# Kernel tuning notes

Measured on AMD Instinct MI355X. Metric: run time of the kernel, lower is better.

The kernel has to match this reference:

```python
import jax, jax.numpy as jnp
import numpy as np

V = 196608   # HEALPix nside=128 pixels
NNZ = 9 * V  # ~8 neighbors + self loop per pixel
B, FIN, FOUT, K = 4, 32, 64, 5


def setup_inputs() -> dict:
    key = jax.random.key(0)
    k1, k2, k3, k4, k5, k6 = jax.random.split(key, 6)
    lap_rows = jax.random.randint(k1, (NNZ,), 0, V, dtype=jnp.int32)
    lap_cols = jax.random.randint(k2, (NNZ,), 0, V, dtype=jnp.int32)
    # scale values so the Chebyshev recurrence stays numerically tame
    lap_vals = jax.random.normal(k3, (NNZ,), dtype=jnp.float32) * 0.1
    inputs = jax.random.normal(k4, (B, V, FIN), dtype=jnp.float32)
    std = np.sqrt(2.0 / (FIN + FOUT)).astype(np.float32)  # xavier normal
    weight = jax.random.normal(k5, (K, FIN, FOUT), dtype=jnp.float32) * std
    bias = jnp.full((FOUT,), 0.01, dtype=jnp.float32)
    return {"lap_rows": lap_rows, "lap_cols": lap_cols, "lap_vals": lap_vals,
            "inputs": inputs, "weight": weight, "bias": bias}


def reference(lap_rows, lap_cols, lap_vals, inputs, weight, bias):
    Bq, Vq, Fin = inputs.shape
    Kq, _, Fout = weight.shape

    # x0: [V, Fin*B]  (matches torch permute(1,2,0).reshape)
    x0 = jnp.transpose(inputs, (1, 2, 0)).reshape(Vq, Fin * Bq)

    def spmm(x):  # sparse [V,V] @ dense [V, Fin*B] via gather + scatter-add
        contrib = lap_vals[:, None] * x[lap_cols]  # [nnz, Fin*B]
        return jax.ops.segment_sum(contrib, lap_rows, num_segments=Vq)

    xs = [x0]
    if Kq > 1:
        xs.append(spmm(x0))
    for _ in range(2, Kq):
        xs.append(2.0 * spmm(xs[-1]) - xs[-2])
    cheb = jnp.stack(xs)  # [K, V, Fin*B]

    # [K,V,Fin,B] -> [B,V,Fin,K] -> [B*V, Fin*K]
    cheb = cheb.reshape(Kq, Vq, Fin, Bq).transpose(3, 1, 2, 0).reshape(Bq * Vq, Fin * Kq)
    # torch weight.view(Fin*K, Fout) flattens (K,Fin) row-major -> reshape(K*Fin, Fout)
    w2 = weight.reshape(Kq * Fin, Fout)
    out = (cheb @ w2).reshape(Bq, Vq, Fout)
    return out + bias
```

## Files before the change

### kernel.cpp

```cpp
#include <hip/hip_runtime.h>

#define V 196608
#define NNZ (9 * V)
#define B 4
#define FIN 32
#define FOUT 64
#define K 5
#define C 128
#define ROWU 64
#define SPMM_BLOCKS 2048

typedef __attribute__((ext_vector_type(8))) short bf16x8;
typedef __attribute__((ext_vector_type(4))) float f32x4;

static __device__ __forceinline__ unsigned int f2bf(float f) {
    union { float f; unsigned int u; } v; v.f = f;
    return (v.u + 0x7FFFu + ((v.u >> 16) & 1u)) >> 16;
}
static __device__ __forceinline__ float bflo(unsigned int u) {
    union { unsigned int u; float f; } v; v.u = u << 16; return v.f;
}
static __device__ __forceinline__ float bfhi(unsigned int u) {
    union { unsigned int u; float f; } v; v.u = u & 0xFFFF0000u; return v.f;
}

__global__ void zero_cursor(uint4* __restrict__ p) {
    int t = blockIdx.x * 256 + threadIdx.x;
    if (t < V / 4) p[t] = (uint4){0u, 0u, 0u, 0u};
}

__global__ void build_x0(const float* __restrict__ inp, unsigned int* __restrict__ x0) {
    int t = blockIdx.x * 256 + threadIdx.x;
    if (t >= V * 64) return;
    int d = t & 63;
    int v = t >> 6;
    int b = d >> 4;
    int fin = (d & 15) * 2;
    const float* s = inp + ((size_t)b * V + v) * 32 + fin;
    float f0 = s[0], f1 = s[1];
    x0[(size_t)v * ROWU + d] = f2bf(f0) | (f2bf(f1) << 16);
}

__global__ void build_wfrag(const float* __restrict__ w, uint4* __restrict__ wfh,
                            uint4* __restrict__ wfl) {
    int idx = blockIdx.x * 256 + threadIdx.x;
    if (idx >= K * 4 * 64) return;
    int lane = idx & 63;
    int nt = (idx >> 6) & 3;
    int k = idx >> 8;
    int col = lane & 15;
    int quad = lane >> 4;
    int o = nt * 16 + col;
    unsigned int hh[8], ll[8];
#pragma unroll
    for (int e = 0; e < 8; ++e) {
        int fin = quad * 8 + e;
        float wv = w[(fin * 5 + k) * 64 + o];
        unsigned int hb = f2bf(wv);
        float hf = bflo(hb);
        ll[e] = f2bf(wv - hf);
        hh[e] = hb;
    }
    uint4 uh, ul;
    uh.x = hh[0] | (hh[1] << 16);
    uh.y = hh[2] | (hh[3] << 16);
    uh.z = hh[4] | (hh[5] << 16);
    uh.w = hh[6] | (hh[7] << 16);
    ul.x = ll[0] | (ll[1] << 16);
    ul.y = ll[2] | (ll[3] << 16);
    ul.z = ll[4] | (ll[5] << 16);
    ul.w = ll[6] | (ll[7] << 16);
    wfh[idx] = uh;
    wfl[idx] = ul;
}

__global__ void hist_rows(const int* __restrict__ rows, int* __restrict__ cnt) {
    int e = blockIdx.x * 256 + threadIdx.x;
    if (e < NNZ) atomicAdd(&cnt[rows[e]], 1);
}

__global__ void chunk_sums(const int* __restrict__ cnt, int* __restrict__ bsum) {
    __shared__ int ws[16];
    int tid = threadIdx.x;
    int lane = tid & 63;
    int wid = tid >> 6;
    int v = cnt[blockIdx.x * 1024 + tid];
#pragma unroll
    for (int off = 32; off >= 1; off >>= 1) v += __shfl_down(v, off, 64);
    if (lane == 0) ws[wid] = v;
    __syncthreads();
    if (tid < 16) {
        int s = ws[tid];
#pragma unroll
        for (int off = 8; off >= 1; off >>= 1) s += __shfl_down(s, off, 16);
        if (tid == 0) bsum[blockIdx.x] = s;
    }
}

__global__ void scan_sums(const int* __restrict__ bsum, int* __restrict__ bpre,
                          int* __restrict__ rowptr) {
    __shared__ int ws[4];
    int tid = threadIdx.x;
    int lane = tid & 63;
    int wid = tid >> 6;
    int v = (tid < 192) ? bsum[tid] : 0;
    int x = v;
#pragma unroll
    for (int off = 1; off < 64; off <<= 1) {
        int t = __shfl_up(x, off, 64);
        if (lane >= off) x += t;
    }
    if (lane == 63) ws[wid] = x;
    __syncthreads();
    if (wid == 0 && lane < 4) {
        int s = ws[lane];
        int y = s;
#pragma unroll
        for (int off = 1; off < 4; off <<= 1) {
            int t = __shfl_up(y, off, 4);
            if (lane >= off) y += t;
        }
        ws[lane] = y - s;
    }
    __syncthreads();
    int incl = x + ws[wid];
    if (tid < 192) bpre[tid] = incl - v;
    if (tid == 191) rowptr[V] = incl;
}

__global__ void scan_chunks(const int* __restrict__ cnt, const int* __restrict__ bpre,
                            int* __restrict__ rowptr, int* __restrict__ cursor) {
    __shared__ int wsum[16];
    int tid = threadIdx.x;
    int lane = tid & 63;
    int wid = tid >> 6;
    int base = blockIdx.x * 1024;
    int v = cnt[base + tid];
    int x = v;
#pragma unroll
    for (int off = 1; off < 64; off <<= 1) {
        int t = __shfl_up(x, off, 64);
        if (lane >= off) x += t;
    }
    if (lane == 63) wsum[wid] = x;
    __syncthreads();
    if (wid == 0 && lane < 16) {
        int s = wsum[lane];
        int y = s;
#pragma unroll
        for (int off = 1; off < 16; off <<= 1) {
            int t = __shfl_up(y, off, 16);
            if (lane >= off) y += t;
        }
        wsum[lane] = y - s;
    }
    __syncthreads();
    int excl = x - v + wsum[wid] + bpre[blockIdx.x];
    rowptr[base + tid] = excl;
    cursor[base + tid] = excl;
}

__global__ void scatter_edges_win(const int* __restrict__ rows, const int* __restrict__ cols,
                                  const float* __restrict__ vals, int* __restrict__ cursor,
                                  int2* __restrict__ cev, int lo, int hi) {
    int e = blockIdx.x * 256 + threadIdx.x;
    if (e >= NNZ) return;
    int r = rows[e];
    if (r < lo || r >= hi) return;
    int p = atomicAdd(&cursor[r], 1);
    int2 pk;
    pk.x = cols[e];
    pk.y = __float_as_int(vals[e]);
    cev[p] = pk;
}

template <int COMBINE>
__global__ __launch_bounds__(256) void spmm_gather(
    const int* __restrict__ rowptr, const int2* __restrict__ cev,
    const unsigned int* __restrict__ x, const unsigned int* __restrict__ xm2,
    unsigned int* __restrict__ y) {
    const int lane = threadIdx.x & 63;
    const int wid0 = (blockIdx.x * 256 + threadIdx.x) >> 6;
    const int NW = SPMM_BLOCKS * 4;
    for (int base = wid0 * 2; base < V; base += NW * 2) {
        const int r0 = base, r1 = base + 1;
        const int s0 = rowptr[r0];
        const int e0 = rowptr[r0 + 1];
        const int e1 = rowptr[r1 + 1];
        float ax0 = 0.f, ay0 = 0.f, ax1 = 0.f, ay1 = 0.f;
        int i0 = s0, i1 = e0;
        while (e0 - i0 >= 4 && e1 - i1 >= 4) {
            int2 Ea[4], Eb[4];
#pragma unroll
            for (int j = 0; j < 4; ++j) {
                Ea[j] = cev[i0 + j];
                Eb[j] = cev[i1 + j];
            }
            unsigned int Ua[4], Ub[4];
#pragma unroll
            for (int j = 0; j < 4; ++j) {
                Ua[j] = x[(size_t)Ea[j].x * ROWU + lane];
                Ub[j] = x[(size_t)Eb[j].x * ROWU + lane];
            }
#pragma unroll
            for (int j = 0; j < 4; ++j) {
                float va = __int_as_float(Ea[j].y);
                float vb = __int_as_float(Eb[j].y);
                ax0 = fmaf(va, bflo(Ua[j]), ax0);
                ay0 = fmaf(va, bfhi(Ua[j]), ay0);
                ax1 = fmaf(vb, bflo(Ub[j]), ax1);
                ay1 = fmaf(vb, bfhi(Ub[j]), ay1);
            }
            i0 += 4;
            i1 += 4;
        }
        for (; i0 + 2 <= e0; i0 += 2) {
            int2 a = cev[i0], b = cev[i0 + 1];
            unsigned int u0 = x[(size_t)a.x * ROWU + lane];
            unsigned int u1 = x[(size_t)b.x * ROWU + lane];
            float v0 = __int_as_float(a.y), v1 = __int_as_float(b.y);
            ax0 = fmaf(v0, bflo(u0), ax0);
            ay0 = fmaf(v0, bfhi(u0), ay0);
            ax0 = fmaf(v1, bflo(u1), ax0);
            ay0 = fmaf(v1, bfhi(u1), ay0);
        }
        for (; i0 < e0; ++i0) {
            int2 a = cev[i0];
            unsigned int u = x[(size_t)a.x * ROWU + lane];
            float v = __int_as_float(a.y);
            ax0 = fmaf(v, bflo(u), ax0);
            ay0 = fmaf(v, bfhi(u), ay0);
        }
        for (; i1 + 2 <= e1; i1 += 2) {
            int2 a = cev[i1], b = cev[i1 + 1];
            unsigned int u0 = x[(size_t)a.x * ROWU + lane];
            unsigned int u1 = x[(size_t)b.x * ROWU + lane];
            float v0 = __int_as_float(a.y), v1 = __int_as_float(b.y);
            ax1 = fmaf(v0, bflo(u0), ax1);
            ay1 = fmaf(v0, bfhi(u0), ay1);
            ax1 = fmaf(v1, bflo(u1), ax1);
            ay1 = fmaf(v1, bfhi(u1), ay1);
        }
        for (; i1 < e1; ++i1) {
            int2 a = cev[i1];
            unsigned int u = x[(size_t)a.x * ROWU + lane];
            float v = __int_as_float(a.y);
            ax1 = fmaf(v, bflo(u), ax1);
            ay1 = fmaf(v, bfhi(u), ay1);
        }
        if (COMBINE) {
            unsigned int m0 = xm2[(size_t)r0 * ROWU + lane];
            unsigned int m1 = xm2[(size_t)r1 * ROWU + lane];
            ax0 = 2.0f * ax0 - bflo(m0);
            ay0 = 2.0f * ay0 - bfhi(m0);
            ax1 = 2.0f * ax1 - bflo(m1);
            ay1 = 2.0f * ay1 - bfhi(m1);
        }
        y[(size_t)r0 * ROWU + lane] = f2bf(ax0) | (f2bf(ay0) << 16);
        y[(size_t)r1 * ROWU + lane] = f2bf(ax1) | (f2bf(ay1) << 16);
    }
}

__global__ __launch_bounds__(256) void fused_mfma(
    const unsigned short* __restrict__ x0, const unsigned short* __restrict__ x1,
    const unsigned short* __restrict__ x2, const unsigned short* __restrict__ x3,
    const unsigned short* __restrict__ x4, const uint4* __restrict__ wfh,
    const uint4* __restrict__ wfl, const float* __restrict__ bias,
    float* __restrict__ out) {
    const int tid = threadIdx.x;
    const int lane = tid & 63;
    const int g = (blockIdx.x * 256 + tid) >> 6;
    const int v0 = g << 4;
    const int col = lane & 15;
    const int quad = lane >> 4;
    const unsigned short* const xs[K] = {x0, x1, x2, x3, x4};

    f32x4 acc[B][4];
#pragma unroll
    for (int b = 0; b < B; ++b)
#pragma unroll
        for (int nt = 0; nt < 4; ++nt) acc[b][nt] = (f32x4){0.f, 0.f, 0.f, 0.f};

#pragma unroll
    for (int k = 0; k < K; ++k) {
        const unsigned short* xk = xs[k] + ((size_t)(v0 + col)) * C + quad * 8;
        bf16x8 a0 = *reinterpret_cast<const bf16x8*>(xk);
        bf16x8 a1 = *reinterpret_cast<const bf16x8*>(xk + 32);
        bf16x8 a2 = *reinterpret_cast<const bf16x8*>(xk + 64);
        bf16x8 a3 = *reinterpret_cast<const bf16x8*>(xk + 96);
#pragma unroll
        for (int nt = 0; nt < 4; ++nt) {
            uint4 uh = wfh[(k * 4 + nt) * 64 + lane];
            uint4 ul = wfl[(k * 4 + nt) * 64 + lane];
            bf16x8 wh = *reinterpret_cast<bf16x8*>(&uh);
            bf16x8 wl = *reinterpret_cast<bf16x8*>(&ul);
            acc[0][nt] = __builtin_amdgcn_mfma_f32_16x16x32_bf16(a0, wh, acc[0][nt], 0, 0, 0);
            acc[1][nt] = __builtin_amdgcn_mfma_f32_16x16x32_bf16(a1, wh, acc[1][nt], 0, 0, 0);
            acc[2][nt] = __builtin_amdgcn_mfma_f32_16x16x32_bf16(a2, wh, acc[2][nt], 0, 0, 0);
            acc[3][nt] = __builtin_amdgcn_mfma_f32_16x16x32_bf16(a3, wh, acc[3][nt], 0, 0, 0);
            acc[0][nt] = __builtin_amdgcn_mfma_f32_16x16x32_bf16(a0, wl, acc[0][nt], 0, 0, 0);
            acc[1][nt] = __builtin_amdgcn_mfma_f32_16x16x32_bf16(a1, wl, acc[1][nt], 0, 0, 0);
            acc[2][nt] = __builtin_amdgcn_mfma_f32_16x16x32_bf16(a2, wl, acc[2][nt], 0, 0, 0);
            acc[3][nt] = __builtin_amdgcn_mfma_f32_16x16x32_bf16(a3, wl, acc[3][nt], 0, 0, 0);
        }
    }

    float bv[4];
#pragma unroll
    for (int nt = 0; nt < 4; ++nt) bv[nt] = bias[nt * 16 + col];
#pragma unroll
    for (int b = 0; b < B; ++b)
#pragma unroll
        for (int nt = 0; nt < 4; ++nt)
#pragma unroll
            for (int r = 0; r < 4; ++r) {
                int row = quad * 4 + r;
                out[((size_t)b * V + v0 + row) * FOUT + nt * 16 + col] = acc[b][nt][r] + bv[nt];
            }
}

extern "C" void kernel_launch(void* const* d_in, const int* in_sizes, int n_in,
                              void* d_out, int out_size, void* d_ws, size_t ws_size,
                              hipStream_t stream) {
    const int* lap_rows = (const int*)d_in[0];
    const int* lap_cols = (const int*)d_in[1];
    const float* lap_vals = (const float*)d_in[2];
    const float* inputs = (const float*)d_in[3];
    const float* weight = (const float*)d_in[4];
    const float* bias = (const float*)d_in[5];
    float* out = (float*)d_out;

    char* p = (char*)d_ws;
    auto alloc = [&](size_t bytes) {
        char* r = p;
        p += (bytes + 511) & ~(size_t)511;
        return r;
    };
    int* rowptr = (int*)alloc((size_t)(V + 1) * 4);
    int* cursor = (int*)alloc((size_t)V * 4);
    int* bsum = (int*)alloc(192 * 4);
    int* bpre = (int*)alloc(192 * 4);
    uint4* wfh = (uint4*)alloc((size_t)K * 4 * 64 * 16);
    uint4* wfl = (uint4*)alloc((size_t)K * 4 * 64 * 16);
    int2* cev = (int2*)alloc((size_t)NNZ * 8);
    unsigned int* xb0 = (unsigned int*)alloc((size_t)V * ROWU * 4);
    unsigned int* xb1 = (unsigned int*)alloc((size_t)V * ROWU * 4);
    unsigned int* xb2 = (unsigned int*)alloc((size_t)V * ROWU * 4);
    unsigned int* xb3 = (unsigned int*)alloc((size_t)V * ROWU * 4);
    unsigned int* xb4 = (unsigned int*)alloc((size_t)V * ROWU * 4);

    const int edge_blocks = (NNZ + 255) / 256;
    const int x0_blocks = (V * 64) / 256;
    const int mfma_blocks = (V / 16) * 64 / 256;

    zero_cursor<<<(V / 4 + 255) / 256, 256, 0, stream>>>((uint4*)cursor);
    hist_rows<<<edge_blocks, 256, 0, stream>>>(lap_rows, cursor);
    chunk_sums<<<V / 1024, 1024, 0, stream>>>(cursor, bsum);
    scan_sums<<<1, 256, 0, stream>>>(bsum, bpre, rowptr);
    scan_chunks<<<V / 1024, 1024, 0, stream>>>(cursor, bpre, rowptr, cursor);
    for (int w = 0; w < 4; ++w) {
        scatter_edges_win<<<edge_blocks, 256, 0, stream>>>(
            lap_rows, lap_cols, lap_vals, cursor, cev, w * (V / 4), (w + 1) * (V / 4));
    }

    build_x0<<<x0_blocks, 256, 0, stream>>>(inputs, xb0);
    build_wfrag<<<5, 256, 0, stream>>>(weight, wfh, wfl);

    spmm_gather<0><<<SPMM_BLOCKS, 256, 0, stream>>>(rowptr, cev, xb0, nullptr, xb1);
    spmm_gather<1><<<SPMM_BLOCKS, 256, 0, stream>>>(rowptr, cev, xb1, xb0, xb2);
    spmm_gather<1><<<SPMM_BLOCKS, 256, 0, stream>>>(rowptr, cev, xb2, xb1, xb3);
    spmm_gather<1><<<SPMM_BLOCKS, 256, 0, stream>>>(rowptr, cev, xb3, xb2, xb4);

    fused_mfma<<<mfma_blocks, 256, 0, stream>>>(
        (const unsigned short*)xb0, (const unsigned short*)xb1, (const unsigned short*)xb2,
        (const unsigned short*)xb3, (const unsigned short*)xb4, wfh, wfl, bias, out);
}
```

Measured before the change: 652.1 us.

## Partition SpMM work by equal nonzero ranges with binary-searched row bounds

Replaces the fixed two-rows-per-wave SpMM with a merge-path style kernel. Each wave gets a contiguous nnz range, locates its row bounds by binary search over rowptr, and streams edges eight at a time, flushing rows as boundaries pass. The aim is to balance work across waves, stream the edge array contiguously and keep eight gathers in flight. It adds binary-search overhead per wave and per-edge row-boundary checks.

```diff
diff --git a/kernel.cpp b/kernel.cpp
--- a/kernel.cpp
+++ b/kernel.cpp
@@ -175,89 +175,88 @@
 }
 
 template <int COMBINE>
-__global__ __launch_bounds__(256) void spmm_gather(
+__global__ __launch_bounds__(256) void spmm_seg(
     const int* __restrict__ rowptr, const int2* __restrict__ cev,
     const unsigned int* __restrict__ x, const unsigned int* __restrict__ xm2,
     unsigned int* __restrict__ y) {
     const int lane = threadIdx.x & 63;
-    const int wid0 = (blockIdx.x * 256 + threadIdx.x) >> 6;
+    const int w = (blockIdx.x * 256 + threadIdx.x) >> 6;
     const int NW = SPMM_BLOCKS * 4;
-    for (int base = wid0 * 2; base < V; base += NW * 2) {
-        const int r0 = base, r1 = base + 1;
-        const int s0 = rowptr[r0];
-        const int e0 = rowptr[r0 + 1];
-        const int e1 = rowptr[r1 + 1];
-        float ax0 = 0.f, ay0 = 0.f, ax1 = 0.f, ay1 = 0.f;
-        int i0 = s0, i1 = e0;
-        while (e0 - i0 >= 4 && e1 - i1 >= 4) {
-            int2 Ea[4], Eb[4];
-#pragma unroll
-            for (int j = 0; j < 4; ++j) {
-                Ea[j] = cev[i0 + j];
-                Eb[j] = cev[i1 + j];
+    const int lo = (int)((long long)NNZ * w / NW);
+    const int hi = (int)((long long)NNZ * (w + 1) / NW);
+    int a = 0, b = V;
+    while (a < b) {
+        int m = (a + b) >> 1;
+        if (rowptr[m] < lo) a = m + 1; else b = m;
+    }
+    int r = a;
+    int rend;
+    if (w == NW - 1) {
+        rend = V;
+    } else {
+        a = r; b = V;
+        while (a < b) {
+            int m = (a + b) >> 1;
+            if (rowptr[m] < hi) a = m + 1; else b = m;
+        }
+        rend = a;
+    }
+    if (r >= rend) return;
+    int i = rowptr[r];
+    const int e = rowptr[rend];
+    int nb = rowptr[r + 1];
+    float ax = 0.f, ay = 0.f;
+
+    auto flushrow = [&](int row) {
+        float ox = ax, oy = ay;
+        if (COMBINE) {
+            unsigned int m0 = xm2[(size_t)row * ROWU + lane];
+            ox = 2.f * ox - bflo(m0);
+            oy = 2.f * oy - bfhi(m0);
+        }
+        y[(size_t)row * ROWU + lane] = f2bf(ox) | (f2bf(oy) << 16);
+        ax = 0.f;
+        ay = 0.f;
+    };
+
+    while (i < e) {
+        if (e - i >= 8) {
+            int2 E8[8];
+#pragma unroll
+            for (int t = 0; t < 8; ++t) E8[t] = cev[i + t];
+            unsigned int U8[8];
+#pragma unroll
+            for (int t = 0; t < 8; ++t) U8[t] = x[(size_t)E8[t].x * ROWU + lane];
+#pragma unroll
+            for (int t = 0; t < 8; ++t) {
+                int cur = i + t;
+                while (cur == nb) {
+                    flushrow(r);
+                    ++r;
+                    nb = rowptr[r + 1];
+                }
+                float v = __int_as_float(E8[t].y);
+                ax = fmaf(v, bflo(U8[t]), ax);
+                ay = fmaf(v, bfhi(U8[t]), ay);
             }
-            unsigned int Ua[4], Ub[4];
-#pragma unroll
-            for (int j = 0; j < 4; ++j) {
-                Ua[j] = x[(size_t)Ea[j].x * ROWU + lane];
-                Ub[j] = x[(size_t)Eb[j].x * ROWU + lane];
+            i += 8;
+        } else {
+            int2 ev = cev[i];
+            unsigned int u = x[(size_t)ev.x * ROWU + lane];
+            while (i == nb) {
+                flushrow(r);
+                ++r;
+                nb = rowptr[r + 1];
             }
-#pragma unroll
-            for (int j = 0; j < 4; ++j) {
-                float va = __int_as_float(Ea[j].y);
-                float vb = __int_as_float(Eb[j].y);
-                ax0 = fmaf(va, bflo(Ua[j]), ax0);
-                ay0 = fmaf(va, bfhi(Ua[j]), ay0);
-                ax1 = fmaf(vb, bflo(Ub[j]), ax1);
-                ay1 = fmaf(vb, bfhi(Ub[j]), ay1);
-            }
-            i0 += 4;
-            i1 += 4;
-        }
-        for (; i0 + 2 <= e0; i0 += 2) {
-            int2 a = cev[i0], b = cev[i0 + 1];
-            unsigned int u0 = x[(size_t)a.x * ROWU + lane];
-            unsigned int u1 = x[(size_t)b.x * ROWU + lane];
-            float v0 = __int_as_float(a.y), v1 = __int_as_float(b.y);
-            ax0 = fmaf(v0, bflo(u0), ax0);
-            ay0 = fmaf(v0, bfhi(u0), ay0);
-            ax0 = fmaf(v1, bflo(u1), ax0);
-            ay0 = fmaf(v1, bfhi(u1), ay0);
-        }
-        for (; i0 < e0; ++i0) {
-            int2 a = cev[i0];
-            unsigned int u = x[(size_t)a.x * ROWU + lane];
-            float v = __int_as_float(a.y);
-            ax0 = fmaf(v, bflo(u), ax0);
-            ay0 = fmaf(v, bfhi(u), ay0);
-        }
-        for (; i1 + 2 <= e1; i1 += 2) {
-            int2 a = cev[i1], b = cev[i1 + 1];
-            unsigned int u0 = x[(size_t)a.x * ROWU + lane];
-            unsigned int u1 = x[(size_t)b.x * ROWU + lane];
-            float v0 = __int_as_float(a.y), v1 = __int_as_float(b.y);
-            ax1 = fmaf(v0, bflo(u0), ax1);
-            ay1 = fmaf(v0, bfhi(u0), ay1);
-            ax1 = fmaf(v1, bflo(u1), ax1);
-            ay1 = fmaf(v1, bfhi(u1), ay1);
-        }
-        for (; i1 < e1; ++i1) {
-            int2 a = cev[i1];
-            unsigned int u = x[(size_t)a.x * ROWU + lane];
-            float v = __int_as_float(a.y);
-            ax1 = fmaf(v, bflo(u), ax1);
-            ay1 = fmaf(v, bfhi(u), ay1);
-        }
-        if (COMBINE) {
-            unsigned int m0 = xm2[(size_t)r0 * ROWU + lane];
-            unsigned int m1 = xm2[(size_t)r1 * ROWU + lane];
-            ax0 = 2.0f * ax0 - bflo(m0);
-            ay0 = 2.0f * ay0 - bfhi(m0);
-            ax1 = 2.0f * ax1 - bflo(m1);
-            ay1 = 2.0f * ay1 - bfhi(m1);
-        }
-        y[(size_t)r0 * ROWU + lane] = f2bf(ax0) | (f2bf(ay0) << 16);
-        y[(size_t)r1 * ROWU + lane] = f2bf(ax1) | (f2bf(ay1) << 16);
+            float v = __int_as_float(ev.y);
+            ax = fmaf(v, bflo(u), ax);
+            ay = fmaf(v, bfhi(u), ay);
+            ++i;
+        }
+    }
+    while (r < rend) {
+        flushrow(r);
+        ++r;
     }
 }
 
@@ -366,10 +365,10 @@
     build_x0<<<x0_blocks, 256, 0, stream>>>(inputs, xb0);
     build_wfrag<<<5, 256, 0, stream>>>(weight, wfh, wfl);
 
-    spmm_gather<0><<<SPMM_BLOCKS, 256, 0, stream>>>(rowptr, cev, xb0, nullptr, xb1);
-    spmm_gather<1><<<SPMM_BLOCKS, 256, 0, stream>>>(rowptr, cev, xb1, xb0, xb2);
-    spmm_gather<1><<<SPMM_BLOCKS, 256, 0, stream>>>(rowptr, cev, xb2, xb1, xb3);
-    spmm_gather<1><<<SPMM_BLOCKS, 256, 0, stream>>>(rowptr, cev, xb3, xb2, xb4);
+    spmm_seg<0><<<SPMM_BLOCKS, 256, 0, stream>>>(rowptr, cev, xb0, nullptr, xb1);
+    spmm_seg<1><<<SPMM_BLOCKS, 256, 0, stream>>>(rowptr, cev, xb1, xb0, xb2);
+    spmm_seg<1><<<SPMM_BLOCKS, 256, 0, stream>>>(rowptr, cev, xb2, xb1, xb3);
+    spmm_seg<1><<<SPMM_BLOCKS, 256, 0, stream>>>(rowptr, cev, xb3, xb2, xb4);
 
     fused_mfma<<<mfma_blocks, 256, 0, stream>>>(
         (const unsigned short*)xb0, (const unsigned short*)xb1, (const unsigned short*)xb2,
```

New measurement: 666.5 us. 2.2% more time.

## Fuse final Chebyshev SpMM into MFMA GEMM kernel via LDS staging

Applied to the files above, without the earlier changes.

The last SpMM step (x4 = 2*L*x3 - x2) now runs inside the GEMM kernel. Each wave gathers its 16 rows into a swizzled LDS tile and feeds them straight to the MFMA for k=4. This drops one kernel launch and the global write and re-read of the x4 buffer. Separately, build_x0 now uses vectorized float4 loads and uint4 stores. The trade-off is that the gather's latency is now serialized with the GEMM in the same kernel, and LDS use could lower occupancy.

```diff
diff --git a/kernel.cpp b/kernel.cpp
--- a/kernel.cpp
+++ b/kernel.cpp
@@ -29,16 +29,21 @@
     if (t < V / 4) p[t] = (uint4){0u, 0u, 0u, 0u};
 }
 
-__global__ void build_x0(const float* __restrict__ inp, unsigned int* __restrict__ x0) {
+__global__ void build_x0(const float* __restrict__ inp, uint4* __restrict__ x0v) {
     int t = blockIdx.x * 256 + threadIdx.x;
-    if (t >= V * 64) return;
-    int d = t & 63;
-    int v = t >> 6;
-    int b = d >> 4;
-    int fin = (d & 15) * 2;
-    const float* s = inp + ((size_t)b * V + v) * 32 + fin;
-    float f0 = s[0], f1 = s[1];
-    x0[(size_t)v * ROWU + d] = f2bf(f0) | (f2bf(f1) << 16);
+    if (t >= V * 16) return;
+    int v = t >> 4;
+    int seg = t & 15;
+    int b = seg >> 2;
+    int q = seg & 3;
+    const float4* s = reinterpret_cast<const float4*>(inp + ((size_t)b * V + v) * 32 + q * 8);
+    float4 fa = s[0], fb = s[1];
+    uint4 u;
+    u.x = f2bf(fa.x) | (f2bf(fa.y) << 16);
+    u.y = f2bf(fa.z) | (f2bf(fa.w) << 16);
+    u.z = f2bf(fb.x) | (f2bf(fb.y) << 16);
+    u.w = f2bf(fb.z) | (f2bf(fb.w) << 16);
+    x0v[(size_t)v * 16 + seg] = u;
 }
 
 __global__ void build_wfrag(const float* __restrict__ w, uint4* __restrict__ wfh,
@@ -262,18 +267,80 @@
 }
 
 __global__ __launch_bounds__(256) void fused_mfma(
-    const unsigned short* __restrict__ x0, const unsigned short* __restrict__ x1,
-    const unsigned short* __restrict__ x2, const unsigned short* __restrict__ x3,
-    const unsigned short* __restrict__ x4, const uint4* __restrict__ wfh,
-    const uint4* __restrict__ wfl, const float* __restrict__ bias,
-    float* __restrict__ out) {
+    const unsigned int* __restrict__ x0, const unsigned int* __restrict__ x1,
+    const unsigned int* __restrict__ x2, const unsigned int* __restrict__ x3,
+    const int* __restrict__ rowptr, const int2* __restrict__ cev,
+    const uint4* __restrict__ wfh, const uint4* __restrict__ wfl,
+    const float* __restrict__ bias, float* __restrict__ out) {
+    __shared__ unsigned int lx4[64 * 64];
     const int tid = threadIdx.x;
     const int lane = tid & 63;
-    const int g = (blockIdx.x * 256 + tid) >> 6;
-    const int v0 = g << 4;
+    const int wid = tid >> 6;
+    const int gv0 = blockIdx.x * 64;
+    const int wv0 = gv0 + wid * 16;
+
+    for (int p = 0; p < 8; ++p) {
+        const int r0 = wv0 + 2 * p, r1 = r0 + 1;
+        const int s0 = rowptr[r0];
+        const int e0 = rowptr[r0 + 1];
+        const int e1 = rowptr[r1 + 1];
+        float ax0 = 0.f, ay0 = 0.f, ax1 = 0.f, ay1 = 0.f;
+        int i0 = s0, i1 = e0;
+        while (e0 - i0 >= 4 && e1 - i1 >= 4) {
+            int2 Ea[4], Eb[4];
+#pragma unroll
+            for (int j = 0; j < 4; ++j) {
+                Ea[j] = cev[i0 + j];
+                Eb[j] = cev[i1 + j];
+            }
+            unsigned int Ua[4], Ub[4];
+#pragma unroll
+            for (int j = 0; j < 4; ++j) {
+                Ua[j] = x3[(size_t)Ea[j].x * ROWU + lane];
+                Ub[j] = x3[(size_t)Eb[j].x * ROWU + lane];
+            }
+#pragma unroll
+            for (int j = 0; j < 4; ++j) {
+                float va = __int_as_float(Ea[j].y);
+                float vb = __int_as_float(Eb[j].y);
+                ax0 = fmaf(va, bflo(Ua[j]), ax0);
+                ay0 = fmaf(va, bfhi(Ua[j]), ay0);
+                ax1 = fmaf(vb, bflo(Ub[j]), ax1);
+                ay1 = fmaf(vb, bfhi(Ub[j]), ay1);
+            }
+            i0 += 4;
+            i1 += 4;
+        }
+        for (; i0 < e0; ++i0) {
+            int2 a = cev[i0];
+            unsigned int u = x3[(size_t)a.x * ROWU + lane];
+            float v = __int_as_float(a.y);
+            ax0 = fmaf(v, bflo(u), ax0);
+            ay0 = fmaf(v, bfhi(u), ay0);
+        }
+        for (; i1 < e1; ++i1) {
+            int2 a = cev[i1];
+            unsigned int u = x3[(size_t)a.x * ROWU + lane];
+            float v = __int_as_float(a.y);
+            ax1 = fmaf(v, bflo(u), ax1);
+            ay1 = fmaf(v, bfhi(u), ay1);
+        }
+        unsigned int m0 = x2[(size_t)r0 * ROWU + lane];
+        unsigned int m1 = x2[(size_t)r1 * ROWU + lane];
+        ax0 = 2.0f * ax0 - bflo(m0);
+        ay0 = 2.0f * ay0 - bfhi(m0);
+        ax1 = 2.0f * ax1 - bflo(m1);
+        ay1 = 2.0f * ay1 - bfhi(m1);
+        const int lr0 = wid * 16 + 2 * p, lr1 = lr0 + 1;
+        lx4[(lr0 << 6) + ((lane + lr0 * 4) & 63)] = f2bf(ax0) | (f2bf(ay0) << 16);
+        lx4[(lr1 << 6) + ((lane + lr1 * 4) & 63)] = f2bf(ax1) | (f2bf(ay1) << 16);
+    }
+
+    const int v0 = wv0;
     const int col = lane & 15;
     const int quad = lane >> 4;
-    const unsigned short* const xs[K] = {x0, x1, x2, x3, x4};
+    const unsigned int* const xs[4] = {x0, x1, x2, x3};
+    const int lr = wid * 16 + col;
 
     f32x4 acc[B][4];
 #pragma unroll
@@ -283,11 +350,24 @@
 
 #pragma unroll
     for (int k = 0; k < K; ++k) {
-        const unsigned short* xk = xs[k] + ((size_t)(v0 + col)) * C + quad * 8;
-        bf16x8 a0 = *reinterpret_cast<const bf16x8*>(xk);
-        bf16x8 a1 = *reinterpret_cast<const bf16x8*>(xk + 32);
-        bf16x8 a2 = *reinterpret_cast<const bf16x8*>(xk + 64);
-        bf16x8 a3 = *reinterpret_cast<const bf16x8*>(xk + 96);
+        bf16x8 a0, a1, a2, a3;
+        if (k < 4) {
+            const unsigned short* xk =
+                reinterpret_cast<const unsigned short*>(xs[k]) + ((size_t)(v0 + col)) * C + quad * 8;
+            a0 = *reinterpret_cast<const bf16x8*>(xk);
+            a1 = *reinterpret_cast<const bf16x8*>(xk + 32);
+            a2 = *reinterpret_cast<const bf16x8*>(xk + 64);
+            a3 = *reinterpret_cast<const bf16x8*>(xk + 96);
+        } else {
+            uint4 u0 = *reinterpret_cast<const uint4*>(&lx4[(lr << 6) + ((0 * 16 + quad * 4 + lr * 4) & 63)]);
+            uint4 u1 = *reinterpret_cast<const uint4*>(&lx4[(lr << 6) + ((1 * 16 + quad * 4 + lr * 4) & 63)]);
+            uint4 u2 = *reinterpret_cast<const uint4*>(&lx4[(lr << 6) + ((2 * 16 + quad * 4 + lr * 4) & 63)]);
+            uint4 u3 = *reinterpret_cast<const uint4*>(&lx4[(lr << 6) + ((3 * 16 + quad * 4 + lr * 4) & 63)]);
+            a0 = *reinterpret_cast<bf16x8*>(&u0);
+            a1 = *reinterpret_cast<bf16x8*>(&u1);
+            a2 = *reinterpret_cast<bf16x8*>(&u2);
+            a3 = *reinterpret_cast<bf16x8*>(&u3);
+        }
 #pragma unroll
         for (int nt = 0; nt < 4; ++nt) {
             uint4 uh = wfh[(k * 4 + nt) * 64 + lane];
@@ -347,11 +427,10 @@
     unsigned int* xb1 = (unsigned int*)alloc((size_t)V * ROWU * 4);
     unsigned int* xb2 = (unsigned int*)alloc((size_t)V * ROWU * 4);
     unsigned int* xb3 = (unsigned int*)alloc((size_t)V * ROWU * 4);
-    unsigned int* xb4 = (unsigned int*)alloc((size_t)V * ROWU * 4);
 
     const int edge_blocks = (NNZ + 255) / 256;
-    const int x0_blocks = (V * 64) / 256;
-    const int mfma_blocks = (V / 16) * 64 / 256;
+    const int x0_blocks = (V * 16 + 255) / 256;
+    const int mfma_blocks = V / 64;
 
     zero_cursor<<<(V / 4 + 255) / 256, 256, 0, stream>>>((uint4*)cursor);
     hist_rows<<<edge_blocks, 256, 0, stream>>>(lap_rows, cursor);
@@ -363,15 +442,13 @@
             lap_rows, lap_cols, lap_vals, cursor, cev, w * (V / 4), (w + 1) * (V / 4));
     }
 
-    build_x0<<<x0_blocks, 256, 0, stream>>>(inputs, xb0);
+    build_x0<<<x0_blocks, 256, 0, stream>>>(inputs, (uint4*)xb0);
     build_wfrag<<<5, 256, 0, stream>>>(weight, wfh, wfl);
 
     spmm_gather<0><<<SPMM_BLOCKS, 256, 0, stream>>>(rowptr, cev, xb0, nullptr, xb1);
     spmm_gather<1><<<SPMM_BLOCKS, 256, 0, stream>>>(rowptr, cev, xb1, xb0, xb2);
     spmm_gather<1><<<SPMM_BLOCKS, 256, 0, stream>>>(rowptr, cev, xb2, xb1, xb3);
-    spmm_gather<1><<<SPMM_BLOCKS, 256, 0, stream>>>(rowptr, cev, xb3, xb2, xb4);
-
-    fused_mfma<<<mfma_blocks, 256, 0, stream>>>(
-        (const unsigned short*)xb0, (const unsigned short*)xb1, (const unsigned short*)xb2,
-        (const unsigned short*)xb3, (const unsigned short*)xb4, wfh, wfl, bias, out);
-}
+
+    fused_mfma<<<mfma_blocks, 256, 0, stream>>>(xb0, xb1, xb2, xb3, rowptr, cev,
+                                                wfh, wfl, bias, out);
+}
```

Measured after the change: 734.7 us. +12.7%, slower.
